# Performance work log

Measured on AMD Instinct MI355X. Metric: run time of the kernel, lower is better.

## Reference

```python
import jax, jax.numpy as jnp
import numpy as np

L, D, NH, DH, K = 2, 128, 4, 32, 3  # blocks, latent_dim, heads, head_dim, kernel

def _ln(x, eps=1e-6):
    mu = x.mean(-1, keepdims=True)
    var = x.var(-1, keepdims=True)
    return (x - mu) / jnp.sqrt(var + eps)

def setup_inputs() -> dict:
    key = jax.random.key(0)
    ks = jax.random.split(key, 12)
    B, Hd, Wd = 2, 64, 96
    s = 0.02
    p = lambda k, shape: jax.random.normal(k, shape, jnp.float32) * s
    return {
        'feat_map': jax.random.normal(ks[0], (B, D, Hd, Wd), jnp.float32),
        'feat_map_up': jax.random.normal(ks[1], (B, D, 2 * Hd, 2 * Wd), jnp.float32),
        'nc_w': jnp.ones((L, D), jnp.float32), 'nc_b': jnp.zeros((L, D), jnp.float32),
        'wq': p(ks[2], (L, D, D)), 'bq': jnp.zeros((L, D), jnp.float32),
        'wkv': p(ks[3], (L, D, 2 * D)), 'bkv': jnp.zeros((L, 2 * D), jnp.float32),
        'wo': p(ks[4], (L, D, D)), 'bo': jnp.zeros((L, D), jnp.float32),
        'w1': p(ks[5], (L, D, 4 * D)), 'b1': jnp.zeros((L, 4 * D), jnp.float32),
        'w2': p(ks[6], (L, 4 * D, D)), 'b2': jnp.zeros((L, D), jnp.float32),
        'wqf': p(ks[7], (D, D)), 'bqf': jnp.zeros((D,), jnp.float32),
        'wcf': p(ks[8], (D, D)), 'bcf': jnp.zeros((D,), jnp.float32),
        'upsample_factor': 2,
    }

def reference(feat_map, feat_map_up, nc_w, nc_b, wq, bq, wkv, bkv, wo, bo,
              w1, b1, w2, b2, wqf, bqf, wcf, bcf, upsample_factor):
    B, C, Hd, Wd = feat_map.shape
    Hu, Wu = Hd * upsample_factor, Wd * upsample_factor
    N = B * Hu * Wu
    # ---- local 3x3 context via replicate-pad + shifted slices (== pad+unfold) ----
    pad = jnp.pad(feat_map, ((0, 0), (0, 0), (1, 1), (1, 1)), mode='edge')
    patches = jnp.stack([pad[:, :, i:i + Hd, j:j + Wd]
                         for i in range(K) for j in range(K)], axis=2)  # [B,C,9,Hd,Wd]
    # nearest-neighbor upsample by factor (== F.interpolate nearest)
    patches = jnp.repeat(jnp.repeat(patches, upsample_factor, axis=-2),
                         upsample_factor, axis=-1)                      # [B,C,9,Hu,Wu]
    context = patches.transpose(0, 3, 4, 2, 1).reshape(N, K * K, C)     # [(b h w),9,C]
    x = feat_map_up.transpose(0, 2, 3, 1).reshape(N, 1, C)              # [(b h w),1,C]
    scale = 1.0 / float(np.sqrt(DH))
    for l in range(L):
        # cross-attn: x = x + Attn(norm1(x), norm_ctx(context))
        ctx_n = _ln(context) * nc_w[l] + nc_b[l]
        q = _ln(x) @ wq[l] + bq[l]
        kv = ctx_n @ wkv[l] + bkv[l]
        k_, v_ = kv[..., :D], kv[..., D:]
        qh = q.reshape(N, 1, NH, DH).transpose(0, 2, 1, 3)       # [N,h,1,dh]
        kh = k_.reshape(N, K * K, NH, DH).transpose(0, 2, 1, 3)  # [N,h,9,dh]
        vh = v_.reshape(N, K * K, NH, DH).transpose(0, 2, 1, 3)
        attn = jax.nn.softmax(jnp.einsum('nhqd,nhkd->nhqk', qh, kh) * scale, axis=-1)
        o = jnp.einsum('nhqk,nhkd->nhqd', attn, vh).transpose(0, 2, 1, 3).reshape(N, 1, D)
        x = x + (o @ wo[l] + bo[l])
        # MLP: x = x + W2 gelu(W1 norm2(x))
        h = jax.nn.gelu(_ln(x) @ w1[l] + b1[l])  # tanh-approx gelu
        x = x + (h @ w2[l] + b2[l])
    # ---- final query-context attention mask ----
    xq = _ln(x) @ wqf + bqf
    ctxp = _ln(context) @ wcf + bcf
    logits = jnp.einsum('nqc,nkc->nqk', xq, ctxp) * (1.0 / float(np.sqrt(D)))
    attn_mask = jax.nn.softmax(logits, axis=-1)              # [N,1,9]
    return attn_mask.reshape(B, Hu, Wu, K * K).transpose(0, 3, 1, 2)  # [B,9,Hu,Wu]
```

## Files before the change

kernel.cpp:

```cpp
#include <hip/hip_runtime.h>

namespace {

constexpr int THREADS = 256;
constexpr int HdC = 64, WdC = 96, HuC = 128, WuC = 192;


__device__ __forceinline__ float gelu_tanh(float x) {
  float z = 0.7978845608028654f * (x + 0.044715f * x * x * x);
  float e = __expf(2.0f * z);
  float t = 1.0f - 2.0f / (e + 1.0f);
  return 0.5f * x * (1.0f + t);
}

__device__ __forceinline__ unsigned short f2bf(float f) {
  unsigned int u = __builtin_bit_cast(unsigned int, f);
  u = (u + 0x7FFFu + ((u >> 16) & 1u)) >> 16;
  return (unsigned short)u;
}

__device__ __forceinline__ float bf2f(unsigned short u) {
  unsigned int x = ((unsigned int)u) << 16;
  return __builtin_bit_cast(float, x);
}
// ... 357 lines not shown
          FMA_ROW(xd + 0, a0, w);
          FMA_ROW(xd + 4, a1, w);
          FMA_ROW(xd + 8, a2, w);
          FMA_ROW(xd + 12, a3, w);
        }
      }
    }
    {
      const float4 bv = *reinterpret_cast<const float4*>(b2 + l * 128 + col0);
#pragma unroll
      for (int i = 0; i < 4; ++i) {
        float* xr = sm.xs + (row0 + i) * XS_S + col0;
        float4 x = *reinterpret_cast<float4*>(xr);
        x.x += xd[i * 4 + 0] + bv.x; x.y += xd[i * 4 + 1] + bv.y;
        x.z += xd[i * 4 + 2] + bv.z; x.w += xd[i * 4 + 3] + bv.w;
        *reinterpret_cast<float4*>(xr) = x;
      }
    }
    __syncthreads();
  }

  layernorm_x(sm.xs, sm.xnT, sm.scratch, tid);
  gemm32(wqf, 128, sm.xnT, sm.wbuf, tid, acc);
  {
    const float4 bv = *reinterpret_cast<const float4*>(bqf + col0);
#pragma unroll
    for (int i = 0; i < 4; ++i) {
      float4 o;
      o.x = acc[i * 4 + 0] + bv.x; o.y = acc[i * 4 + 1] + bv.y;
      o.z = acc[i * 4 + 2] + bv.z; o.w = acc[i * 4 + 3] + bv.w;
      *reinterpret_cast<float4*>(sm.outb + (row0 + i) * OB_S + col0) = o;
    }
  }
  gemm96<false>(wcf, 128, sm.ctxT, sm.wbuf, sm.kvb, bcf, nullptr, tid);
  __syncthreads();
  {
    const int px = tid >> 3, sub = tid & 7;
    const int lr = (((px >> 3) >> 1) << 2) | ((px & 7) >> 1);
    const float* qrow = sm.outb + px * OB_S;
    {
      const float* crow = sm.kvb + (lr * 9 + sub) * KV_S;
      float s = 0.f;
#pragma unroll 8
      for (int c = 0; c < 128; c += 4) {
        const float4 qv = *reinterpret_cast<const float4*>(qrow + c);
        const float4 cv = *reinterpret_cast<const float4*>(crow + c);
        s += qv.x * cv.x + qv.y * cv.y + qv.z * cv.z + qv.w * cv.w;
      }
      sm.scratch[SC_LG + px * 12 + sub] = s;
    }
    if (sub == 0) {
      const float* crow = sm.kvb + (lr * 9 + 8) * KV_S;
      float s = 0.f;
#pragma unroll 8
      for (int c = 0; c < 128; c += 4) {
        const float4 qv = *reinterpret_cast<const float4*>(qrow + c);
        const float4 cv = *reinterpret_cast<const float4*>(crow + c);
        s += qv.x * cv.x + qv.y * cv.y + qv.z * cv.z + qv.w * cv.w;
      }
      sm.scratch[SC_LG + px * 12 + 8] = s;
    }
  }
  __syncthreads();
  if (tid < 32) {
    const int px = tid;
    const int hu = hu0 + (px >> 3), wu = wu0 + (px & 7);
    float lg[9], mx = -1e30f;
#pragma unroll
    for (int kk = 0; kk < 9; ++kk) {
      lg[kk] = sm.scratch[SC_LG + px * 12 + kk] * 0.08838834764831845f;
      mx = fmaxf(mx, lg[kk]);
    }
    float sum = 0.f;
#pragma unroll
    for (int kk = 0; kk < 9; ++kk) { lg[kk] = __expf(lg[kk] - mx); sum += lg[kk]; }
    const float inv = 1.f / sum;
#pragma unroll
    for (int kk = 0; kk < 9; ++kk)
      out[((bz * 9 + kk) * HuC + hu) * WuC + wu] = lg[kk] * inv;
  }
}


constexpr int PANEL = 16384;
constexpr int N_PANELS = 26;
constexpr size_t WS_NEEDED = (size_t)N_PANELS * PANEL * 2 + 2048;
constexpr int CBS = 136;
constexpr int XTS = 132;

constexpr int MSC_ATT = 0;
constexpr int MSC_LN  = 1152;
constexpr int MSC_ST  = 1408;
constexpr int MSC_N   = 1472;

typedef __attribute__((ext_vector_type(8))) short bf16x8;
typedef __attribute__((ext_vector_type(4))) float f32x4;
typedef __attribute__((ext_vector_type(8))) unsigned short u16x8;

struct alignas(16) SmemM {
  unsigned short ctxn[80 * CBS];
  unsigned short kvb[80 * CBS];
  unsigned short xn[32 * CBS];
  unsigned short hb[32 * CBS];
  unsigned short outb[32 * CBS];
  float scratch[MSC_N];
};
static_assert(sizeof(SmemM) <= 80 * 1024, "LDS budget (need 2 blocks/CU)");

__global__ void prep_weights(
    const float* __restrict__ nc_w, const float* __restrict__ nc_b,
    const float* __restrict__ wq, const float* __restrict__ wkv,
    const float* __restrict__ bkv,
    const float* __restrict__ wo, const float* __restrict__ w1,
    const float* __restrict__ w2, const float* __restrict__ wqf,
    const float* __restrict__ wcf,
    unsigned short* __restrict__ wsp, float* __restrict__ wsb) {
  const int b = blockIdx.x;
  const int t = threadIdx.x;
  if (b >= 104) {
    const int l = b - 104;
    float acc = bkv[l * 256 + t];
    for (int k = 0; k < 128; ++k)
      acc += nc_b[l * 128 + k] * wkv[l * 32768 + k * 256 + t];
    wsb[l * 256 + t] = acc;
    return;
  }
  const int pid = b >> 2, qtr = b & 3;
  const float* src = wqf; int N = 128, koff = 0, noff = 0;
  const float* sc = nullptr;
  if (pid < 24) {
    const int l = pid / 12, loc = pid % 12;
    if (loc == 0)      { src = wq + l * 16384;  N = 128; }
    else if (loc == 1) { src = wkv + l * 32768; N = 256; sc = nc_w + l * 128; }
    else if (loc == 2) { src = wkv + l * 32768; N = 256; noff = 128; sc = nc_w + l * 128; }
    else if (loc == 3) { src = wo + l * 16384;  N = 128; }
    else if (loc < 8)  { src = w1 + l * 65536;  N = 512; noff = (loc - 4) * 128; }
    else               { src = w2 + l * 65536;  N = 128; koff = (loc - 8) * 128; }
  } else if (pid == 25) { src = wcf; }
  unsigned short* dst = wsp + pid * PANEL;
#pragma unroll
  for (int p = 0; p < 2; ++p) {
    const int e = t + p * 256;
    const int n = e & 127;
    const int kg = e >> 7;
    const int k0 = qtr * 32 + kg * 8;
    unsigned short tmp[8];
#pragma unroll
    for (int i = 0; i < 8; ++i) {
      const float s = sc ? sc[k0 + i] : 1.f;
      tmp[i] = f2bf(src[(k0 + i + koff) * N + noff + n] * s);
    }
    *reinterpret_cast<u16x8*>(dst + n * 128 + k0) = *reinterpret_cast<u16x8*>(tmp);
  }
}

__device__ __forceinline__ void load_b8(const unsigned short* __restrict__ W,
                                        bf16x8 b[2][4], int nl, int q8, int w2t) {
#pragma unroll
  for (int t = 0; t < 2; ++t)
#pragma unroll
    for (int ks = 0; ks < 4; ++ks)
      b[t][ks] = *reinterpret_cast<const bf16x8*>(
          W + ((w2t + t) * 16 + nl) * 128 + ks * 32 + q8);
}

__device__ __forceinline__ void mfma32v(const unsigned short* A, const bf16x8 b[2][4],
                                        f32x4 acc[4], int nl, int q8, bool init) {
  if (init) {
#pragma unroll
    for (int i = 0; i < 4; ++i) acc[i] = (f32x4){0.f, 0.f, 0.f, 0.f};
  }
#pragma unroll
  for (int ks = 0; ks < 4; ++ks) {
    const bf16x8 a0 = *reinterpret_cast<const bf16x8*>(A + nl * CBS + ks * 32 + q8);
    const bf16x8 a1 = *reinterpret_cast<const bf16x8*>(A + (16 + nl) * CBS + ks * 32 + q8);
    acc[0] = __builtin_amdgcn_mfma_f32_16x16x32_bf16(a0, b[0][ks], acc[0], 0, 0, 0);
    acc[1] = __builtin_amdgcn_mfma_f32_16x16x32_bf16(a0, b[1][ks], acc[1], 0, 0, 0);
    acc[2] = __builtin_amdgcn_mfma_f32_16x16x32_bf16(a1, b[0][ks], acc[2], 0, 0, 0);
    acc[3] = __builtin_amdgcn_mfma_f32_16x16x32_bf16(a1, b[1][ks], acc[3], 0, 0, 0);
  }
}

__device__ __forceinline__ void mfma72v(const unsigned short* Ctx, const bf16x8 b[2][4],
                                        f32x4 acc[10], int nl, int q8) {
#pragma unroll
  for (int i = 0; i < 10; ++i) acc[i] = (f32x4){0.f, 0.f, 0.f, 0.f};
#pragma unroll
  for (int ks = 0; ks < 4; ++ks) {
    const bf16x8 b0 = b[0][ks], b1 = b[1][ks];
#pragma unroll
    for (int rt = 0; rt < 5; ++rt) {
      const bf16x8 a = *reinterpret_cast<const bf16x8*>(
          Ctx + (rt * 16 + nl) * CBS + ks * 32 + q8);
      acc[rt * 2 + 0] = __builtin_amdgcn_mfma_f32_16x16x32_bf16(a, b0, acc[rt * 2 + 0], 0, 0, 0);
      acc[rt * 2 + 1] = __builtin_amdgcn_mfma_f32_16x16x32_bf16(a, b1, acc[rt * 2 + 1], 0, 0, 0);
    }
  }
}

__device__ __forceinline__ void ln_x(const float (&xr)[2][2][4], unsigned short* xn,
                                     float* scratch, int wave, int nl, int qm) {
#pragma unroll
  for (int rt = 0; rt < 2; ++rt)
#pragma unroll
    for (int r = 0; r < 4; ++r) {
      float s1 = xr[rt][0][r] + xr[rt][1][r];
      float s2 = xr[rt][0][r] * xr[rt][0][r] + xr[rt][1][r] * xr[rt][1][r];
#pragma unroll
      for (int m = 1; m < 16; m <<= 1) {
        s1 += __shfl_xor(s1, m, 64);
        s2 += __shfl_xor(s2, m, 64);
      }
      if (nl == 0) {
        const int px = rt * 16 + qm + r;
        scratch[MSC_LN + px * 4 + wave] = s1;
        scratch[MSC_LN + 128 + px * 4 + wave] = s2;
      }
    }
  __syncthreads();
#pragma unroll
  for (int rt = 0; rt < 2; ++rt)
#pragma unroll
    for (int r = 0; r < 4; ++r) {
      const int px = rt * 16 + qm + r;
      float a = 0.f, b = 0.f;
#pragma unroll
      for (int w = 0; w < 4; ++w) {
        a += scratch[MSC_LN + px * 4 + w];
        b += scratch[MSC_LN + 128 + px * 4 + w];
      }
      const float m = a * (1.f / 128.f);
      const float v = b * (1.f / 128.f) - m * m;
      const float rs = rsqrtf(v + 1e-6f);
#pragma unroll
      for (int t = 0; t < 2; ++t)
        xn[px * CBS + (wave * 2 + t) * 16 + nl] = f2bf((xr[rt][t][r] - m) * rs);
    }
  __syncthreads();
}

__global__ __launch_bounds__(THREADS, 2) void fused_interp_mfma(
    const float* __restrict__ fm, const float* __restrict__ fmu,
    const float* __restrict__ bq, const float* __restrict__ bo,
    const float* __restrict__ b1, const float* __restrict__ b2,
    const float* __restrict__ bqf, const float* __restrict__ bcf,
    const unsigned short* __restrict__ wsp, const float* __restrict__ wsb,
    float* __restrict__ out) {
  __shared__ SmemM sm;
  const int tid = threadIdx.x;
  const int bx = blockIdx.x, by = blockIdx.y, bz = blockIdx.z;
  const int lh0 = by * 2, lw0 = bx * 4;
  const int hu0 = by * 4, wu0 = bx * 8;

  const int lane = tid & 63;
  const int wave = tid >> 6;
  const int nl = lane & 15;
  const int q8 = (lane >> 4) * 8;
  const int qm = (lane >> 4) * 4;
  const int w2t = wave * 2;

  {
    float* xtmp = reinterpret_cast<float*>(sm.ctxn);
#pragma unroll
    for (int p = 0; p < 8; ++p) {
      const int e = tid + p * THREADS;
      const int pe = e & 15;
      const int c = e >> 4;
      const int hu = hu0 + (pe >> 2);
      const int wu = wu0 + (pe & 3) * 2;
      const float2 v = *reinterpret_cast<const float2*>(
          &fmu[((bz * 128 + c) * HuC + hu) * WuC + wu]);
      const int px = (pe >> 2) * 8 + (pe & 3) * 2;
      xtmp[px * XTS + c] = v.x;
      xtmp[(px + 1) * XTS + c] = v.y;
    }
  }
  __syncthreads();
  float xr[2][2][4];
  {
    const float* xtmp = reinterpret_cast<const float*>(sm.ctxn);
#pragma unroll
    for (int rt = 0; rt < 2; ++rt)
#pragma unroll
      for (int t = 0; t < 2; ++t)
#pragma unroll
        for (int r = 0; r < 4; ++r)
          xr[rt][t][r] = xtmp[(rt * 16 + qm + r) * XTS + (w2t + t) * 16 + nl];
  }
  __syncthreads();

  {
    float* patch = reinterpret_cast<float*>(sm.kvb);
#pragma unroll
    for (int p = 0; p < 12; ++p) {
      const int e = tid + p * THREADS;
      const int c = e / 24;
      const int rem = e - c * 24;
      const int hs_i = rem / 6;
      const int ws_i = rem - hs_i * 6;
      int hd = lh0 - 1 + hs_i; hd = hd < 0 ? 0 : (hd > HdC - 1 ? HdC - 1 : hd);
      int wd = lw0 - 1 + ws_i; wd = wd < 0 ? 0 : (wd > WdC - 1 ? WdC - 1 : wd);
      patch[(hs_i * 6 + ws_i) * XTS + c] = fm[((bz * 128 + c) * HdC + hd) * WdC + wd];
    }
  }
  __syncthreads();
  {
    const float* patch = reinterpret_cast<const float*>(sm.kvb);
    if (tid < 192) {
      const int pp = tid >> 3, part = tid & 7;
      float s1 = 0.f, s2 = 0.f;
#pragma unroll
      for (int i = 0; i < 16; ++i) {
        const float v = patch[pp * XTS + part * 16 + i];
        s1 += v; s2 += v * v;
      }
      sm.scratch[MSC_ATT + tid * 2 + 0] = s1;
      sm.scratch[MSC_ATT + tid * 2 + 1] = s2;
    }
    __syncthreads();
    if (tid < 24) {
      float a = 0.f, b = 0.f;
#pragma unroll
      for (int g = 0; g < 8; ++g) {
        a += sm.scratch[MSC_ATT + (tid * 8 + g) * 2 + 0];
        b += sm.scratch[MSC_ATT + (tid * 8 + g) * 2 + 1];
      }
      const float m = a * (1.f / 128.f);
      const float v = b * (1.f / 128.f) - m * m;
      sm.scratch[MSC_ST + tid * 2 + 0] = m;
      sm.scratch[MSC_ST + tid * 2 + 1] = rsqrtf(v + 1e-6f);
    }
    __syncthreads();
#pragma unroll
    for (int p = 0; p < 5; ++p) {
      const int e = tid + p * THREADS;
      if (e < 1152) {
        const int r = e >> 4, cg = e & 15;
        const int lr = r / 9;
        const int kk = r - lr * 9;
        const int ki = kk / 3, kj = kk - ki * 3;
        const int pp = ((lr >> 2) + ki) * 6 + (lr & 3) + kj;
        const float m = sm.scratch[MSC_ST + pp * 2 + 0];
        const float rs = sm.scratch[MSC_ST + pp * 2 + 1];
        unsigned short tmp[8];
#pragma unroll
        for (int j = 0; j < 8; ++j)
          tmp[j] = f2bf((patch[pp * XTS + cg * 8 + j] - m) * rs);
        *reinterpret_cast<u16x8*>(sm.ctxn + r * CBS + cg * 8) = *reinterpret_cast<u16x8*>(tmp);
      }
    }
  }
  __syncthreads();

  f32x4 acc4[4];
  f32x4 acc10[10];
  bf16x8 Ba[2][4], Bb[2][4];

  for (int l = 0; l < 2; ++l) {
    const unsigned short* P = wsp + (l * 12) * PANEL;

    float kb[2], vb[2], bqr[2], bor[2], b2r[2], b1r[4][2];
#pragma unroll
    for (int t = 0; t < 2; ++t) {
      const int n = (w2t + t) * 16 + nl;
      kb[t] = wsb[l * 256 + n];
      vb[t] = wsb[l * 256 + 128 + n];
      bqr[t] = bq[l * 128 + n];
      bor[t] = bo[l * 128 + n];
      b2r[t] = b2[l * 128 + n];
#pragma unroll
      for (int cc = 0; cc < 4; ++cc) b1r[cc][t] = b1[l * 512 + cc * 128 + n];
    }

    load_b8(P + 0 * PANEL, Ba, nl, q8, w2t);
    load_b8(P + 1 * PANEL, Bb, nl, q8, w2t);
    ln_x(xr, sm.xn, sm.scratch, wave, nl, qm);

    mfma32v(sm.xn, Ba, acc4, nl, q8, true);
#pragma unroll
    for (int rt = 0; rt < 2; ++rt)
#pragma unroll
      for (int t = 0; t < 2; ++t) {
        const int n = (w2t + t) * 16 + nl;
#pragma unroll
        for (int r = 0; r < 4; ++r)
          sm.outb[(rt * 16 + qm + r) * CBS + n] = f2bf(acc4[rt * 2 + t][r] + bqr[t]);
      }
    mfma72v(sm.ctxn, Bb, acc10, nl, q8);
    load_b8(P + 2 * PANEL, Ba, nl, q8, w2t);
#pragma unroll
    for (int t = 0; t < 2; ++t) {
      const int n = (w2t + t) * 16 + nl;
#pragma unroll
      for (int rt = 0; rt < 5; ++rt)
#pragma unroll
        for (int r = 0; r < 4; ++r) {
          const int row = rt * 16 + qm + r;
          if (row < 72) sm.kvb[row * CBS + n] = f2bf(acc10[rt * 2 + t][r] + kb[t]);
        }
    }
    __syncthreads();

    {
      const int u = tid >> 1, sub = tid & 1;
      const int px = u >> 2, h = u & 3;
      const int lr = (((px >> 3) >> 1) << 2) | ((px & 7) >> 1);
      const unsigned short* qrow = sm.outb + px * CBS + h * 32;
      const int base = sub ? 5 : 0;
      const int cnt = sub ? 4 : 5;
      float mine[5];
#pragma unroll
      for (int i = 0; i < 5; ++i) mine[i] = 0.f;
#pragma unroll
      for (int c8 = 0; c8 < 4; ++c8) {
        const u16x8 qa = *reinterpret_cast<const u16x8*>(qrow + c8 * 8);
        float qaf[8];
#pragma unroll
        for (int j = 0; j < 8; ++j) qaf[j] = bf2f(qa[j]);
#pragma unroll
        for (int i = 0; i < 5; ++i) {
          if (i < cnt) {
            const u16x8 ka = *reinterpret_cast<const u16x8*>(
                sm.kvb + (lr * 9 + base + i) * CBS + h * 32 + c8 * 8);
            float s = 0.f;
#pragma unroll
            for (int j = 0; j < 8; ++j) s += qaf[j] * bf2f(ka[j]);
            mine[i] += s;
          }
        }
      }
#pragma unroll
      for (int i = 0; i < 5; ++i) mine[i] *= 0.17677669529663687f;
      float other[5];
#pragma unroll
      for (int i = 0; i < 5; ++i) other[i] = __shfl_xor(mine[i], 1, 64);
      float lg[9];
#pragma unroll
      for (int j = 0; j < 5; ++j) lg[j] = sub ? other[j] : mine[j];
#pragma unroll
      for (int j = 0; j < 4; ++j) lg[5 + j] = sub ? mine[j] : other[j];
      float mx = -1e30f;
#pragma unroll
      for (int kk = 0; kk < 9; ++kk) mx = fmaxf(mx, lg[kk]);
      float sum = 0.f;
#pragma unroll
      for (int kk = 0; kk < 9; ++kk) { lg[kk] = __expf(lg[kk] - mx); sum += lg[kk]; }
      const float inv = 1.f / sum;
#pragma unroll
      for (int j = 0; j < 5; ++j)
        if (j < cnt) sm.scratch[MSC_ATT + (px * 4 + h) * 9 + base + j] = lg[base + j] * inv;
    }
    __syncthreads();

    mfma72v(sm.ctxn, Ba, acc10, nl, q8);
    load_b8(P + 3 * PANEL, Bb, nl, q8, w2t);
#pragma unroll
    for (int t = 0; t < 2; ++t) {
      const int n = (w2t + t) * 16 + nl;
#pragma unroll
      for (int rt = 0; rt < 5; ++rt)
#pragma unroll
        for (int r = 0; r < 4; ++r) {
          const int row = rt * 16 + qm + r;
          if (row < 72) sm.kvb[row * CBS + n] = f2bf(acc10[rt * 2 + t][r] + vb[t]);
        }
    }
    __syncthreads();

    {
      const int px = tid >> 3, cg = tid & 7, c0 = cg * 16;
      const int lr = (((px >> 3) >> 1) << 2) | ((px & 7) >> 1);
      const float* aw = sm.scratch + MSC_ATT + (px * 4 + (cg >> 1)) * 9;
      float o[16];
#pragma unroll
      for (int j = 0; j < 16; ++j) o[j] = 0.f;
#pragma unroll
      for (int kk = 0; kk < 9; ++kk) {
        const float a = aw[kk];
        const unsigned short* vrow = sm.kvb + (lr * 9 + kk) * CBS + c0;
        const u16x8 v0 = *reinterpret_cast<const u16x8*>(vrow);
        const u16x8 v1 = *reinterpret_cast<const u16x8*>(vrow + 8);
#pragma unroll
        for (int j = 0; j < 8; ++j) {
          o[j] += a * bf2f(v0[j]);
          o[8 + j] += a * bf2f(v1[j]);
        }
      }
      unsigned short tmp[16];
#pragma unroll
      for (int j = 0; j < 16; ++j) tmp[j] = f2bf(o[j]);
      *reinterpret_cast<u16x8*>(sm.xn + px * CBS + c0) = *reinterpret_cast<u16x8*>(tmp);
      *reinterpret_cast<u16x8*>(sm.xn + px * CBS + c0 + 8) = *reinterpret_cast<u16x8*>(tmp + 8);
    }
    __syncthreads();

    mfma32v(sm.xn, Bb, acc4, nl, q8, true);
#pragma unroll
    for (int rt = 0; rt < 2; ++rt)
#pragma unroll
      for (int t = 0; t < 2; ++t)
#pragma unroll
        for (int r = 0; r < 4; ++r)
          xr[rt][t][r] += acc4[rt * 2 + t][r] + bor[t];

    load_b8(P + 4 * PANEL, Ba, nl, q8, w2t);
    ln_x(xr, sm.xn, sm.scratch, wave, nl, qm);
    f32x4 xd[4];
    for (int cc = 0; cc < 4; ++cc) {
      mfma32v(sm.xn, Ba, acc4, nl, q8, true);
      load_b8(P + (8 + cc) * PANEL, Bb, nl, q8, w2t);
#pragma unroll
      for (int rt = 0; rt < 2; ++rt)
#pragma unroll
        for (int t = 0; t < 2; ++t) {
          const int n = (w2t + t) * 16 + nl;
#pragma unroll
          for (int r = 0; r < 4; ++r)
            sm.hb[(rt * 16 + qm + r) * CBS + n] =
                f2bf(gelu_tanh(acc4[rt * 2 + t][r] + b1r[cc][t]));
        }
      __syncthreads();
      if (cc < 3) load_b8(P + (5 + cc) * PANEL, Ba, nl, q8, w2t);
      mfma32v(sm.hb, Bb, xd, nl, q8, cc == 0);
      if (cc < 3) __syncthreads();
    }
#pragma unroll
    for (int rt = 0; rt < 2; ++rt)
#pragma unroll
      for (int t = 0; t < 2; ++t)
#pragma unroll
        for (int r = 0; r < 4; ++r)
          xr[rt][t][r] += xd[rt * 2 + t][r] + b2r[t];
  }

  float bqfr[2], bcfr[2];
#pragma unroll
  for (int t = 0; t < 2; ++t) {
    const int n = (w2t + t) * 16 + nl;
    bqfr[t] = bqf[n];
    bcfr[t] = bcf[n];
  }
  load_b8(wsp + 24 * PANEL, Ba, nl, q8, w2t);
  load_b8(wsp + 25 * PANEL, Bb, nl, q8, w2t);
  ln_x(xr, sm.xn, sm.scratch, wave, nl, qm);
  mfma32v(sm.xn, Ba, acc4, nl, q8, true);
#pragma unroll
  for (int rt = 0; rt < 2; ++rt)
#pragma unroll
    for (int t = 0; t < 2; ++t) {
      const int n = (w2t + t) * 16 + nl;
#pragma unroll
      for (int r = 0; r < 4; ++r)
        sm.outb[(rt * 16 + qm + r) * CBS + n] = f2bf(acc4[rt * 2 + t][r] + bqfr[t]);
    }
  mfma72v(sm.ctxn, Bb, acc10, nl, q8);
#pragma unroll
  for (int t = 0; t < 2; ++t) {
    const int n = (w2t + t) * 16 + nl;
#pragma unroll
    for (int rt = 0; rt < 5; ++rt)
#pragma unroll
      for (int r = 0; r < 4; ++r) {
        const int row = rt * 16 + qm + r;
        if (row < 72) sm.kvb[row * CBS + n] = f2bf(acc10[rt * 2 + t][r] + bcfr[t]);
      }
  }
  __syncthreads();
  {
    const int px = tid >> 3, sub = tid & 7;
    const int lr = (((px >> 3) >> 1) << 2) | ((px & 7) >> 1);
    const unsigned short* qrow = sm.outb + px * CBS;
#pragma unroll
    for (int which = 0; which < 2; ++which) {
      if (which == 1 && sub != 0) break;
      const int kk = (which == 0) ? sub : 8;
      const unsigned short* crow = sm.kvb + (lr * 9 + kk) * CBS;
      float s = 0.f;
#pragma unroll
      for (int c8 = 0; c8 < 16; ++c8) {
        const u16x8 qa = *reinterpret_cast<const u16x8*>(qrow + c8 * 8);
        const u16x8 ca = *reinterpret_cast<const u16x8*>(crow + c8 * 8);
#pragma unroll
        for (int j = 0; j < 8; ++j) s += bf2f(qa[j]) * bf2f(ca[j]);
      }
      sm.scratch[MSC_ATT + px * 12 + kk] = s;
    }
  }
  __syncthreads();
  if (tid < 32) {
    const int px = tid;
    const int hu = hu0 + (px >> 3), wu = wu0 + (px & 7);
    float lg[9], mx = -1e30f;
#pragma unroll
    for (int kk = 0; kk < 9; ++kk) {
      lg[kk] = sm.scratch[MSC_ATT + px * 12 + kk] * 0.08838834764831845f;
      mx = fmaxf(mx, lg[kk]);
    }
    float sum = 0.f;
#pragma unroll
    for (int kk = 0; kk < 9; ++kk) { lg[kk] = __expf(lg[kk] - mx); sum += lg[kk]; }
    const float inv = 1.f / sum;
#pragma unroll
    for (int kk = 0; kk < 9; ++kk)
      out[((bz * 9 + kk) * HuC + hu) * WuC + wu] = lg[kk] * inv;
  }
}

}

extern "C" void kernel_launch(void* const* d_in, const int* in_sizes, int n_in,
                              void* d_out, int out_size, void* d_ws, size_t ws_size,
                              hipStream_t stream) {
  const float* fm   = (const float*)d_in[0];
  const float* fmu  = (const float*)d_in[1];
  const float* nc_w = (const float*)d_in[2];
  const float* nc_b = (const float*)d_in[3];
  const float* wq   = (const float*)d_in[4];
  const float* bq   = (const float*)d_in[5];
  const float* wkv  = (const float*)d_in[6];
  const float* bkv  = (const float*)d_in[7];
  const float* wo   = (const float*)d_in[8];
  const float* bo   = (const float*)d_in[9];
  const float* w1   = (const float*)d_in[10];
  const float* b1   = (const float*)d_in[11];
  const float* w2   = (const float*)d_in[12];
  const float* b2   = (const float*)d_in[13];
  const float* wqf  = (const float*)d_in[14];
  const float* bqf  = (const float*)d_in[15];
  const float* wcf  = (const float*)d_in[16];
  const float* bcf  = (const float*)d_in[17];
  float* out = (float*)d_out;

  dim3 grid(24, 32, 2);
  if (ws_size >= WS_NEEDED) {
    unsigned short* wsp = (unsigned short*)d_ws;
    float* wsb = (float*)((char*)d_ws + (size_t)N_PANELS * PANEL * 2);
    prep_weights<<<dim3(106), dim3(256), 0, stream>>>(
        nc_w, nc_b, wq, wkv, bkv, wo, w1, w2, wqf, wcf, wsp, wsb);
    fused_interp_mfma<<<grid, dim3(THREADS), 0, stream>>>(
        fm, fmu, bq, bo, b1, b2, bqf, bcf, wsp, wsb, out);
  } else {
    fused_interp_kernel<<<grid, dim3(THREADS), 0, stream>>>(
        fm, fmu, nc_w, nc_b, wq, bq, wkv, bkv, wo, bo, w1, b1, w2, b2,
        wqf, bqf, wcf, bcf, out);
  }
}
```

Before: 305.5 us.

## Use 8 waves per block with one 16-column tile each in MFMA kernel

```diff
diff --git a/kernel.cpp b/kernel.cpp
--- a/kernel.cpp
+++ b/kernel.cpp
@@ -463,6 +463,7 @@
 }
 
 
+constexpr int TM = 512;
 constexpr int PANEL = 16384;
 constexpr int N_PANELS = 26;
 constexpr size_t WS_NEEDED = (size_t)N_PANELS * PANEL * 2 + 2048;
@@ -471,8 +472,9 @@
 
 constexpr int MSC_ATT = 0;
 constexpr int MSC_LN  = 1152;
-constexpr int MSC_ST  = 1408;
-constexpr int MSC_N   = 1472;
+constexpr int MSC_ST  = 1664;
+constexpr int MSC_MV  = 1712;
+constexpr int MSC_N   = 1776;
 
 typedef __attribute__((ext_vector_type(8))) short bf16x8;
 typedef __attribute__((ext_vector_type(4))) float f32x4;
@@ -535,58 +537,54 @@
   }
 }
 
-__device__ __forceinline__ void load_b8(const unsigned short* __restrict__ W,
-                                        bf16x8 b[2][4], int nl, int q8, int w2t) {
-#pragma unroll
-  for (int t = 0; t < 2; ++t)
-#pragma unroll
-    for (int ks = 0; ks < 4; ++ks)
-      b[t][ks] = *reinterpret_cast<const bf16x8*>(
-          W + ((w2t + t) * 16 + nl) * 128 + ks * 32 + q8);
-}
-
-__device__ __forceinline__ void mfma32v(const unsigned short* A, const bf16x8 b[2][4],
-                                        f32x4 acc[4], int nl, int q8, bool init) {
+__device__ __forceinline__ void load_b4(const unsigned short* __restrict__ W,
+                                        bf16x8 b[4], int nl, int q8, int wt) {
+#pragma unroll
+  for (int ks = 0; ks < 4; ++ks)
+    b[ks] = *reinterpret_cast<const bf16x8*>(
+        W + (wt * 16 + nl) * 128 + ks * 32 + q8);
+}
+
+__device__ __forceinline__ void mfma32s(const unsigned short* A, const bf16x8 b[4],
+                                        f32x4 acc[2], int nl, int q8, bool init) {
   if (init) {
-#pragma unroll
-    for (int i = 0; i < 4; ++i) acc[i] = (f32x4){0.f, 0.f, 0.f, 0.f};
+    acc[0] = (f32x4){0.f, 0.f, 0.f, 0.f};
+    acc[1] = (f32x4){0.f, 0.f, 0.f, 0.f};
   }
 #pragma unroll
   for (int ks = 0; ks < 4; ++ks) {
     const bf16x8 a0 = *reinterpret_cast<const bf16x8*>(A + nl * CBS + ks * 32 + q8);
     const bf16x8 a1 = *reinterpret_cast<const bf16x8*>(A + (16 + nl) * CBS + ks * 32 + q8);
-    acc[0] = __builtin_amdgcn_mfma_f32_16x16x32_bf16(a0, b[0][ks], acc[0], 0, 0, 0);
-    acc[1] = __builtin_amdgcn_mfma_f32_16x16x32_bf16(a0, b[1][ks], acc[1], 0, 0, 0);
-    acc[2] = __builtin_amdgcn_mfma_f32_16x16x32_bf16(a1, b[0][ks], acc[2], 0, 0, 0);
-    acc[3] = __builtin_amdgcn_mfma_f32_16x16x32_bf16(a1, b[1][ks], acc[3], 0, 0, 0);
-  }
-}
-
-__device__ __forceinline__ void mfma72v(const unsigned short* Ctx, const bf16x8 b[2][4],
-                                        f32x4 acc[10], int nl, int q8) {
-#pragma unroll
-  for (int i = 0; i < 10; ++i) acc[i] = (f32x4){0.f, 0.f, 0.f, 0.f};
+    acc[0] = __builtin_amdgcn_mfma_f32_16x16x32_bf16(a0, b[ks], acc[0], 0, 0, 0);
+    acc[1] = __builtin_amdgcn_mfma_f32_16x16x32_bf16(a1, b[ks], acc[1], 0, 0, 0);
+  }
+}
+
+__device__ __forceinline__ void mfma72s(const unsigned short* Ctx, const bf16x8 b[4],
+                                        f32x4 acc[5], int nl, int q8) {
+#pragma unroll
+  for (int i = 0; i < 5; ++i) acc[i] = (f32x4){0.f, 0.f, 0.f, 0.f};
 #pragma unroll
   for (int ks = 0; ks < 4; ++ks) {
-    const bf16x8 b0 = b[0][ks], b1 = b[1][ks];
+    const bf16x8 bk = b[ks];
 #pragma unroll
     for (int rt = 0; rt < 5; ++rt) {
       const bf16x8 a = *reinterpret_cast<const bf16x8*>(
           Ctx + (rt * 16 + nl) * CBS + ks * 32 + q8);
-      acc[rt * 2 + 0] = __builtin_amdgcn_mfma_f32_16x16x32_bf16(a, b0, acc[rt * 2 + 0], 0, 0, 0);
-      acc[rt * 2 + 1] = __builtin_amdgcn_mfma_f32_16x16x32_bf16(a, b1, acc[rt * 2 + 1], 0, 0, 0);
-    }
-  }
-}
-
-__device__ __forceinline__ void ln_x(const float (&xr)[2][2][4], unsigned short* xn,
-                                     float* scratch, int wave, int nl, int qm) {
+      acc[rt] = __builtin_amdgcn_mfma_f32_16x16x32_bf16(a, bk, acc[rt], 0, 0, 0);
+    }
+  }
+}
+
+__device__ __forceinline__ void ln_x8(const float (&xr)[2][4], unsigned short* xn,
+                                      float* scratch, int tid, int wave, int nl,
+                                      int qm, int n) {
 #pragma unroll
   for (int rt = 0; rt < 2; ++rt)
 #pragma unroll
     for (int r = 0; r < 4; ++r) {
-      float s1 = xr[rt][0][r] + xr[rt][1][r];
-      float s2 = xr[rt][0][r] * xr[rt][0][r] + xr[rt][1][r] * xr[rt][1][r];
+      float s1 = xr[rt][r];
+      float s2 = s1 * s1;
 #pragma unroll
       for (int m = 1; m < 16; m <<= 1) {
         s1 += __shfl_xor(s1, m, 64);
@@ -594,33 +592,37 @@
       }
       if (nl == 0) {
         const int px = rt * 16 + qm + r;
-        scratch[MSC_LN + px * 4 + wave] = s1;
-        scratch[MSC_LN + 128 + px * 4 + wave] = s2;
-      }
-    }
+        scratch[MSC_LN + px * 8 + wave] = s1;
+        scratch[MSC_LN + 256 + px * 8 + wave] = s2;
+      }
+    }
+  __syncthreads();
+  if (tid < 32) {
+    float a = 0.f, b = 0.f;
+#pragma unroll
+    for (int w = 0; w < 8; ++w) {
+      a += scratch[MSC_LN + tid * 8 + w];
+      b += scratch[MSC_LN + 256 + tid * 8 + w];
+    }
+    const float m = a * (1.f / 128.f);
+    const float v = b * (1.f / 128.f) - m * m;
+    scratch[MSC_MV + tid * 2 + 0] = m;
+    scratch[MSC_MV + tid * 2 + 1] = rsqrtf(v + 1e-6f);
+  }
   __syncthreads();
 #pragma unroll
   for (int rt = 0; rt < 2; ++rt)
 #pragma unroll
     for (int r = 0; r < 4; ++r) {
       const int px = rt * 16 + qm + r;
-      float a = 0.f, b = 0.f;
-#pragma unroll
-      for (int w = 0; w < 4; ++w) {
-        a += scratch[MSC_LN + px * 4 + w];
-        b += scratch[MSC_LN + 128 + px * 4 + w];
-      }
-      const float m = a * (1.f / 128.f);
-      const float v = b * (1.f / 128.f) - m * m;
-      const float rs = rsqrtf(v + 1e-6f);
-#pragma unroll
-      for (int t = 0; t < 2; ++t)
-        xn[px * CBS + (wave * 2 + t) * 16 + nl] = f2bf((xr[rt][t][r] - m) * rs);
-    }
-  __syncthreads();
-}
-
-__global__ __launch_bounds__(THREADS, 2) void fused_interp_mfma(
+      const float m = scratch[MSC_MV + px * 2 + 0];
+      const float rs = scratch[MSC_MV + px * 2 + 1];
+      xn[px * CBS + n] = f2bf((xr[rt][r] - m) * rs);
+    }
+  __syncthreads();
+}
+
+__global__ __launch_bounds__(TM, 4) void fused_interp_mfma(
     const float* __restrict__ fm, const float* __restrict__ fmu,
     const float* __restrict__ bq, const float* __restrict__ bo,
     const float* __restrict__ b1, const float* __restrict__ b2,
@@ -638,13 +640,14 @@
   const int nl = lane & 15;
   const int q8 = (lane >> 4) * 8;
   const int qm = (lane >> 4) * 4;
-  const int w2t = wave * 2;
+  const int wt = wave;
+  const int n = wt * 16 + nl;
 
   {
     float* xtmp = reinterpret_cast<float*>(sm.ctxn);
 #pragma unroll
-    for (int p = 0; p < 8; ++p) {
-      const int e = tid + p * THREADS;
+    for (int p = 0; p < 4; ++p) {
+      const int e = tid + p * TM;
       const int pe = e & 15;
       const int c = e >> 4;
       const int hu = hu0 + (pe >> 2);
@@ -657,24 +660,22 @@
     }
   }
   __syncthreads();
-  float xr[2][2][4];
+  float xr[2][4];
   {
     const float* xtmp = reinterpret_cast<const float*>(sm.ctxn);
 #pragma unroll
     for (int rt = 0; rt < 2; ++rt)
 #pragma unroll
-      for (int t = 0; t < 2; ++t)
-#pragma unroll
-        for (int r = 0; r < 4; ++r)
-          xr[rt][t][r] = xtmp[(rt * 16 + qm + r) * XTS + (w2t + t) * 16 + nl];
+      for (int r = 0; r < 4; ++r)
+        xr[rt][r] = xtmp[(rt * 16 + qm + r) * XTS + n];
   }
   __syncthreads();
 
   {
     float* patch = reinterpret_cast<float*>(sm.kvb);
 #pragma unroll
-    for (int p = 0; p < 12; ++p) {
-      const int e = tid + p * THREADS;
+    for (int p = 0; p < 6; ++p) {
+      const int e = tid + p * TM;
       const int c = e / 24;
       const int rem = e - c * 24;
       const int hs_i = rem / 6;
@@ -713,8 +714,8 @@
     }
     __syncthreads();
 #pragma unroll
-    for (int p = 0; p < 5; ++p) {
-      const int e = tid + p * THREADS;
+    for (int p = 0; p < 3; ++p) {
+      const int e = tid + p * TM;
       if (e < 1152) {
         const int r = e >> 4, cg = e & 15;
         const int lr = r / 9;
@@ -733,65 +734,53 @@
   }
   __syncthreads();
 
-  f32x4 acc4[4];
-  f32x4 acc10[10];
-  bf16x8 Ba[2][4], Bb[2][4];
+  f32x4 acc2[2];
+  f32x4 acc5[5];
+  bf16x8 Ba[4], Bb[4];
 
   for (int l = 0; l < 2; ++l) {
     const unsigned short* P = wsp + (l * 12) * PANEL;
 
-    float kb[2], vb[2], bqr[2], bor[2], b2r[2], b1r[4][2];
-#pragma unroll
-    for (int t = 0; t < 2; ++t) {
-      const int n = (w2t + t) * 16 + nl;
-      kb[t] = wsb[l * 256 + n];
-      vb[t] = wsb[l * 256 + 128 + n];
-      bqr[t] = bq[l * 128 + n];
-      bor[t] = bo[l * 128 + n];
-      b2r[t] = b2[l * 128 + n];
-#pragma unroll
-      for (int cc = 0; cc < 4; ++cc) b1r[cc][t] = b1[l * 512 + cc * 128 + n];
-    }
-
-    load_b8(P + 0 * PANEL, Ba, nl, q8, w2t);
-    load_b8(P + 1 * PANEL, Bb, nl, q8, w2t);
-    ln_x(xr, sm.xn, sm.scratch, wave, nl, qm);
-
-    mfma32v(sm.xn, Ba, acc4, nl, q8, true);
+    const float kb = wsb[l * 256 + n];
+    const float vb = wsb[l * 256 + 128 + n];
+    const float bqr = bq[l * 128 + n];
+    const float bor = bo[l * 128 + n];
+    const float b2r = b2[l * 128 + n];
+    float b1r[4];
+#pragma unroll
+    for (int cc = 0; cc < 4; ++cc) b1r[cc] = b1[l * 512 + cc * 128 + n];
+
+    load_b4(P + 0 * PANEL, Ba, nl, q8, wt);
+    load_b4(P + 1 * PANEL, Bb, nl, q8, wt);
+    ln_x8(xr, sm.xn, sm.scratch, tid, wave, nl, qm, n);
+
+    mfma32s(sm.xn, Ba, acc2, nl, q8, true);
 #pragma unroll
     for (int rt = 0; rt < 2; ++rt)
 #pragma unroll
-      for (int t = 0; t < 2; ++t) {
-        const int n = (w2t + t) * 16 + nl;
-#pragma unroll
-        for (int r = 0; r < 4; ++r)
-          sm.outb[(rt * 16 + qm + r) * CBS + n] = f2bf(acc4[rt * 2 + t][r] + bqr[t]);
-      }
-    mfma72v(sm.ctxn, Bb, acc10, nl, q8);
-    load_b8(P + 2 * PANEL, Ba, nl, q8, w2t);
-#pragma unroll
-    for (int t = 0; t < 2; ++t) {
-      const int n = (w2t + t) * 16 + nl;
-#pragma unroll
-      for (int rt = 0; rt < 5; ++rt)
-#pragma unroll
-        for (int r = 0; r < 4; ++r) {
-          const int row = rt * 16 + qm + r;
-          if (row < 72) sm.kvb[row * CBS + n] = f2bf(acc10[rt * 2 + t][r] + kb[t]);
-        }
-    }
+      for (int r = 0; r < 4; ++r)
+        sm.outb[(rt * 16 + qm + r) * CBS + n] = f2bf(acc2[rt][r] + bqr);
+    mfma72s(sm.ctxn, Bb, acc5, nl, q8);
+    load_b4(P + 2 * PANEL, Ba, nl, q8, wt);
+#pragma unroll
+    for (int rt = 0; rt < 5; ++rt)
+#pragma unroll
+      for (int r = 0; r < 4; ++r) {
+        const int row = rt * 16 + qm + r;
+        if (row < 72) sm.kvb[row * CBS + n] = f2bf(acc5[rt][r] + kb);
+      }
     __syncthreads();
 
     {
-      const int u = tid >> 1, sub = tid & 1;
+      const int u = tid >> 2, sub = tid & 3;
       const int px = u >> 2, h = u & 3;
       const int lr = (((px >> 3) >> 1) << 2) | ((px & 7) >> 1);
       const unsigned short* qrow = sm.outb + px * CBS + h * 32;
-      const int base = sub ? 5 : 0;
-      const int cnt = sub ? 4 : 5;
-      float mine[5];
-#pragma unroll
-      for (int i = 0; i < 5; ++i) mine[i] = 0.f;
+      const int base = (sub == 0) ? 0 : (1 + 2 * sub);
+      const int cnt = (sub == 0) ? 3 : 2;
+      float mine[3];
+#pragma unroll
+      for (int i = 0; i < 3; ++i) mine[i] = 0.f;
 #pragma unroll
       for (int c8 = 0; c8 < 4; ++c8) {
         const u16x8 qa = *reinterpret_cast<const u16x8*>(qrow + c8 * 8);
@@ -799,7 +788,7 @@
 #pragma unroll
         for (int j = 0; j < 8; ++j) qaf[j] = bf2f(qa[j]);
 #pragma unroll
-        for (int i = 0; i < 5; ++i) {
+        for (int i = 0; i < 3; ++i) {
           if (i < cnt) {
             const u16x8 ka = *reinterpret_cast<const u16x8*>(
                 sm.kvb + (lr * 9 + base + i) * CBS + h * 32 + c8 * 8);
@@ -810,152 +799,116 @@
           }
         }
       }
-#pragma unroll
-      for (int i = 0; i < 5; ++i) mine[i] *= 0.17677669529663687f;
-      float other[5];
-#pragma unroll
-      for (int i = 0; i < 5; ++i) other[i] = __shfl_xor(mine[i], 1, 64);
-      float lg[9];
-#pragma unroll
-      for (int j = 0; j < 5; ++j) lg[j] = sub ? other[j] : mine[j];
-#pragma unroll
-      for (int j = 0; j < 4; ++j) lg[5 + j] = sub ? mine[j] : other[j];
       float mx = -1e30f;
 #pragma unroll
-      for (int kk = 0; kk < 9; ++kk) mx = fmaxf(mx, lg[kk]);
+      for (int i = 0; i < 3; ++i) {
+        mine[i] *= 0.17677669529663687f;
+        if (i < cnt) mx = fmaxf(mx, mine[i]);
+      }
+      mx = fmaxf(mx, __shfl_xor(mx, 1, 64));
+      mx = fmaxf(mx, __shfl_xor(mx, 2, 64));
       float sum = 0.f;
 #pragma unroll
-      for (int kk = 0; kk < 9; ++kk) { lg[kk] = __expf(lg[kk] - mx); sum += lg[kk]; }
+      for (int i = 0; i < 3; ++i) {
+        if (i < cnt) { mine[i] = __expf(mine[i] - mx); sum += mine[i]; }
+      }
+      sum += __shfl_xor(sum, 1, 64);
+      sum += __shfl_xor(sum, 2, 64);
       const float inv = 1.f / sum;
 #pragma unroll
-      for (int j = 0; j < 5; ++j)
-        if (j < cnt) sm.scratch[MSC_ATT + (px * 4 + h) * 9 + base + j] = lg[base + j] * inv;
-    }
-    __syncthreads();
-
-    mfma72v(sm.ctxn, Ba, acc10, nl, q8);
-    load_b8(P + 3 * PANEL, Bb, nl, q8, w2t);
-#pragma unroll
-    for (int t = 0; t < 2; ++t) {
-      const int n = (w2t + t) * 16 + nl;
-#pragma unroll
-      for (int rt = 0; rt < 5; ++rt)
-#pragma unroll
-        for (int r = 0; r < 4; ++r) {
-          const int row = rt * 16 + qm + r;
-          if (row < 72) sm.kvb[row * CBS + n] = f2bf(acc10[rt * 2 + t][r] + vb[t]);
-        }
-    }
+      for (int i = 0; i < 3; ++i)
+        if (i < cnt) sm.scratch[MSC_ATT + (px * 4 + h) * 9 + base + i] = mine[i] * inv;
+    }
+    __syncthreads();
+
+    mfma72s(sm.ctxn, Ba, acc5, nl, q8);
+    load_b4(P + 3 * PANEL, Bb, nl, q8, wt);
+#pragma unroll
+    for (int rt = 0; rt < 5; ++rt)
+#pragma unroll
+      for (int r = 0; r < 4; ++r) {
+        const int row = rt * 16 + qm + r;
+        if (row < 72) sm.kvb[row * CBS + n] = f2bf(acc5[rt][r] + vb);
+      }
     __syncthreads();
 
     {
-      const int px = tid >> 3, cg = tid & 7, c0 = cg * 16;
+      const int px = tid >> 4, cg = tid & 15, c0 = cg * 8;
       const int lr = (((px >> 3) >> 1) << 2) | ((px & 7) >> 1);
-      const float* aw = sm.scratch + MSC_ATT + (px * 4 + (cg >> 1)) * 9;
-      float o[16];
-#pragma unroll
-      for (int j = 0; j < 16; ++j) o[j] = 0.f;
+      const float* aw = sm.scratch + MSC_ATT + (px * 4 + (cg >> 2)) * 9;
+      float o[8];
+#pragma unroll
+      for (int j = 0; j < 8; ++j) o[j] = 0.f;
 #pragma unroll
       for (int kk = 0; kk < 9; ++kk) {
         const float a = aw[kk];
-        const unsigned short* vrow = sm.kvb + (lr * 9 + kk) * CBS + c0;
-        const u16x8 v0 = *reinterpret_cast<const u16x8*>(vrow);
-        const u16x8 v1 = *reinterpret_cast<const u16x8*>(vrow + 8);
-#pragma unroll
-        for (int j = 0; j < 8; ++j) {
-          o[j] += a * bf2f(v0[j]);
-          o[8 + j] += a * bf2f(v1[j]);
-        }
-      }
-      unsigned short tmp[16];
-#pragma unroll
-      for (int j = 0; j < 16; ++j) tmp[j] = f2bf(o[j]);
+        const u16x8 v0 = *reinterpret_cast<const u16x8*>(sm.kvb + (lr * 9 + kk) * CBS + c0);
+#pragma unroll
+        for (int j = 0; j < 8; ++j) o[j] += a * bf2f(v0[j]);
+      }
+      unsigned short tmp[8];
+#pragma unroll
+      for (int j = 0; j < 8; ++j) tmp[j] = f2bf(o[j]);
       *reinterpret_cast<u16x8*>(sm.xn + px * CBS + c0) = *reinterpret_cast<u16x8*>(tmp);
-      *reinterpret_cast<u16x8*>(sm.xn + px * CBS + c0 + 8) = *reinterpret_cast<u16x8*>(tmp + 8);
-    }
-    __syncthreads();
-
-    mfma32v(sm.xn, Bb, acc4, nl, q8, true);
+    }
+    __syncthreads();
+
+    mfma32s(sm.xn, Bb, acc2, nl, q8, true);
 #pragma unroll
     for (int rt = 0; rt < 2; ++rt)
 #pragma unroll
-      for (int t = 0; t < 2; ++t)
+      for (int r = 0; r < 4; ++r)
+        xr[rt][r] += acc2[rt][r] + bor;
+
+    load_b4(P + 4 * PANEL, Ba, nl, q8, wt);
+    ln_x8(xr, sm.xn, sm.scratch, tid, wave, nl, qm, n);
+    f32x4 xd[2];
+    for (int cc = 0; cc < 4; ++cc) {
+      mfma32s(sm.xn, Ba, acc2, nl, q8, true);
+      load_b4(P + (8 + cc) * PANEL, Bb, nl, q8, wt);
+#pragma unroll
+      for (int rt = 0; rt < 2; ++rt)
 #pragma unroll
         for (int r = 0; r < 4; ++r)
-          xr[rt][t][r] += acc4[rt * 2 + t][r] + bor[t];
-
-    load_b8(P + 4 * PANEL, Ba, nl, q8, w2t);
-    ln_x(xr, sm.xn, sm.scratch, wave, nl, qm);
-    f32x4 xd[4];
-    for (int cc = 0; cc < 4; ++cc) {
-      mfma32v(sm.xn, Ba, acc4, nl, q8, true);
-      load_b8(P + (8 + cc) * PANEL, Bb, nl, q8, w2t);
-#pragma unroll
-      for (int rt = 0; rt < 2; ++rt)
-#pragma unroll
-        for (int t = 0; t < 2; ++t) {
-          const int n = (w2t + t) * 16 + nl;
-#pragma unroll
-          for (int r = 0; r < 4; ++r)
-            sm.hb[(rt * 16 + qm + r) * CBS + n] =
-                f2bf(gelu_tanh(acc4[rt * 2 + t][r] + b1r[cc][t]));
-        }
+          sm.hb[(rt * 16 + qm + r) * CBS + n] = f2bf(gelu_tanh(acc2[rt][r] + b1r[cc]));
       __syncthreads();
-      if (cc < 3) load_b8(P + (5 + cc) * PANEL, Ba, nl, q8, w2t);
-      mfma32v(sm.hb, Bb, xd, nl, q8, cc == 0);
+      if (cc < 3) load_b4(P + (5 + cc) * PANEL, Ba, nl, q8, wt);
+      mfma32s(sm.hb, Bb, xd, nl, q8, cc == 0);
       if (cc < 3) __syncthreads();
     }
 #pragma unroll
     for (int rt = 0; rt < 2; ++rt)
 #pragma unroll
-      for (int t = 0; t < 2; ++t)
-#pragma unroll
-        for (int r = 0; r < 4; ++r)
-          xr[rt][t][r] += xd[rt * 2 + t][r] + b2r[t];
-  }
-
-  float bqfr[2], bcfr[2];
-#pragma unroll
-  for (int t = 0; t < 2; ++t) {
-    const int n = (w2t + t) * 16 + nl;
-    bqfr[t] = bqf[n];
-    bcfr[t] = bcf[n];
-  }
-  load_b8(wsp + 24 * PANEL, Ba, nl, q8, w2t);
-  load_b8(wsp + 25 * PANEL, Bb, nl, q8, w2t);
-  ln_x(xr, sm.xn, sm.scratch, wave, nl, qm);
-  mfma32v(sm.xn, Ba, acc4, nl, q8, true);
+      for (int r = 0; r < 4; ++r)
+        xr[rt][r] += xd[rt][r] + b2r;
+  }
+
+  const float bqfr = bqf[n];
+  const float bcfr = bcf[n];
+  load_b4(wsp + 24 * PANEL, Ba, nl, q8, wt);
+  load_b4(wsp + 25 * PANEL, Bb, nl, q8, wt);
+  ln_x8(xr, sm.xn, sm.scratch, tid, wave, nl, qm, n);
+  mfma32s(sm.xn, Ba, acc2, nl, q8, true);
 #pragma unroll
   for (int rt = 0; rt < 2; ++rt)
 #pragma unroll
-    for (int t = 0; t < 2; ++t) {
-      const int n = (w2t + t) * 16 + nl;
-#pragma unroll
-      for (int r = 0; r < 4; ++r)
-        sm.outb[(rt * 16 + qm + r) * CBS + n] = f2bf(acc4[rt * 2 + t][r] + bqfr[t]);
-    }
-  mfma72v(sm.ctxn, Bb, acc10, nl, q8);
-#pragma unroll
-  for (int t = 0; t < 2; ++t) {
-    const int n = (w2t + t) * 16 + nl;
-#pragma unroll
-    for (int rt = 0; rt < 5; ++rt)
-#pragma unroll
-      for (int r = 0; r < 4; ++r) {
-        const int row = rt * 16 + qm + r;
-        if (row < 72) sm.kvb[row * CBS + n] = f2bf(acc10[rt * 2 + t][r] + bcfr[t]);
-      }
-  }
+    for (int r = 0; r < 4; ++r)
+      sm.outb[(rt * 16 + qm + r) * CBS + n] = f2bf(acc2[rt][r] + bqfr);
+  mfma72s(sm.ctxn, Bb, acc5, nl, q8);
+#pragma unroll
+  for (int rt = 0; rt < 5; ++rt)
+#pragma unroll
+    for (int r = 0; r < 4; ++r) {
+      const int row = rt * 16 + qm + r;
+      if (row < 72) sm.kvb[row * CBS + n] = f2bf(acc5[rt][r] + bcfr);
+    }
   __syncthreads();
   {
-    const int px = tid >> 3, sub = tid & 7;
-    const int lr = (((px >> 3) >> 1) << 2) | ((px & 7) >> 1);
-    const unsigned short* qrow = sm.outb + px * CBS;
-#pragma unroll
-    for (int which = 0; which < 2; ++which) {
-      if (which == 1 && sub != 0) break;
-      const int kk = (which == 0) ? sub : 8;
-      const unsigned short* crow = sm.kvb + (lr * 9 + kk) * CBS;
+    const int px = tid >> 4, sub = tid & 15;
+    if (sub < 9) {
+      const int lr = (((px >> 3) >> 1) << 2) | ((px & 7) >> 1);
+      const unsigned short* qrow = sm.outb + px * CBS;
+      const unsigned short* crow = sm.kvb + (lr * 9 + sub) * CBS;
       float s = 0.f;
 #pragma unroll
       for (int c8 = 0; c8 < 16; ++c8) {
@@ -964,7 +917,7 @@
 #pragma unroll
         for (int j = 0; j < 8; ++j) s += bf2f(qa[j]) * bf2f(ca[j]);
       }
-      sm.scratch[MSC_ATT + px * 12 + kk] = s;
+      sm.scratch[MSC_ATT + px * 12 + sub] = s;
     }
   }
   __syncthreads();
@@ -1018,7 +971,7 @@
     float* wsb = (float*)((char*)d_ws + (size_t)N_PANELS * PANEL * 2);
     prep_weights<<<dim3(106), dim3(256), 0, stream>>>(
         nc_w, nc_b, wq, wkv, bkv, wo, w1, w2, wqf, wcf, wsp, wsb);
-    fused_interp_mfma<<<grid, dim3(THREADS), 0, stream>>>(
+    fused_interp_mfma<<<grid, dim3(TM), 0, stream>>>(
         fm, fmu, bq, bo, b1, b2, bqf, bcf, wsp, wsb, out);
   } else {
     fused_interp_kernel<<<grid, dim3(THREADS), 0, stream>>>(
```

Result: slower. 349.4 us (+14.4%).

## Shrink LDS footprint by aliasing buffers to allow three blocks per CU

Applied to the files above, without the earlier changes.

```diff
diff --git a/kernel.cpp b/kernel.cpp
--- a/kernel.cpp
+++ b/kernel.cpp
@@ -470,23 +470,21 @@
 constexpr int XTS = 132;
 
 constexpr int MSC_ATT = 0;
-constexpr int MSC_LN  = 1152;
-constexpr int MSC_ST  = 1408;
-constexpr int MSC_N   = 1472;
+constexpr int MSC_LN  = 0;
+constexpr int MSC_ST  = 1152;
+constexpr int MSC_N   = 1200;
 
 typedef __attribute__((ext_vector_type(8))) short bf16x8;
 typedef __attribute__((ext_vector_type(4))) float f32x4;
 typedef __attribute__((ext_vector_type(8))) unsigned short u16x8;
 
 struct alignas(16) SmemM {
-  unsigned short ctxn[80 * CBS];
-  unsigned short kvb[80 * CBS];
+  unsigned short ctxn[72 * CBS];
+  unsigned short kvb[72 * CBS];
   unsigned short xn[32 * CBS];
-  unsigned short hb[32 * CBS];
-  unsigned short outb[32 * CBS];
   float scratch[MSC_N];
 };
-static_assert(sizeof(SmemM) <= 80 * 1024, "LDS budget (need 2 blocks/CU)");
+static_assert(sizeof(SmemM) <= 53248, "LDS budget (need 3 blocks/CU)");
 
 __global__ void prep_weights(
     const float* __restrict__ nc_w, const float* __restrict__ nc_b,
@@ -571,10 +569,29 @@
     const bf16x8 b0 = b[0][ks], b1 = b[1][ks];
 #pragma unroll
     for (int rt = 0; rt < 5; ++rt) {
+      const int rb = (rt < 4) ? rt * 16 : 56;
       const bf16x8 a = *reinterpret_cast<const bf16x8*>(
-          Ctx + (rt * 16 + nl) * CBS + ks * 32 + q8);
+          Ctx + (rb + nl) * CBS + ks * 32 + q8);
       acc[rt * 2 + 0] = __builtin_amdgcn_mfma_f32_16x16x32_bf16(a, b0, acc[rt * 2 + 0], 0, 0, 0);
       acc[rt * 2 + 1] = __builtin_amdgcn_mfma_f32_16x16x32_bf16(a, b1, acc[rt * 2 + 1], 0, 0, 0);
+    }
+  }
+}
+
+__device__ __forceinline__ void store72(unsigned short* kvb, const f32x4 acc[10],
+                                        const float bias[2], int nl, int qm, int w2t) {
+#pragma unroll
+  for (int t = 0; t < 2; ++t) {
+    const int n = (w2t + t) * 16 + nl;
+#pragma unroll
+    for (int rt = 0; rt < 5; ++rt) {
+      const int rb = (rt < 4) ? rt * 16 : 56;
+#pragma unroll
+      for (int r = 0; r < 4; ++r) {
+        const int row = rb + qm + r;
+        if (rt < 4 || qm + r >= 8)
+          kvb[row * CBS + n] = f2bf(acc[rt * 2 + t][r] + bias[t]);
+      }
     }
   }
 }
@@ -620,7 +637,7 @@
   __syncthreads();
 }
 
-__global__ __launch_bounds__(THREADS, 2) void fused_interp_mfma(
+__global__ __launch_bounds__(THREADS, 3) void fused_interp_mfma(
     const float* __restrict__ fm, const float* __restrict__ fmu,
     const float* __restrict__ bq, const float* __restrict__ bo,
     const float* __restrict__ b1, const float* __restrict__ b2,
@@ -758,6 +775,10 @@
     ln_x(xr, sm.xn, sm.scratch, wave, nl, qm);
 
     mfma32v(sm.xn, Ba, acc4, nl, q8, true);
+    mfma72v(sm.ctxn, Bb, acc10, nl, q8);
+    load_b8(P + 2 * PANEL, Ba, nl, q8, w2t);
+    store72(sm.kvb, acc10, kb, nl, qm, w2t);
+    __syncthreads();
 #pragma unroll
     for (int rt = 0; rt < 2; ++rt)
 #pragma unroll
@@ -765,28 +786,15 @@
         const int n = (w2t + t) * 16 + nl;
 #pragma unroll
         for (int r = 0; r < 4; ++r)
-          sm.outb[(rt * 16 + qm + r) * CBS + n] = f2bf(acc4[rt * 2 + t][r] + bqr[t]);
-      }
-    mfma72v(sm.ctxn, Bb, acc10, nl, q8);
-    load_b8(P + 2 * PANEL, Ba, nl, q8, w2t);
-#pragma unroll
-    for (int t = 0; t < 2; ++t) {
-      const int n = (w2t + t) * 16 + nl;
-#pragma unroll
-      for (int rt = 0; rt < 5; ++rt)
-#pragma unroll
-        for (int r = 0; r < 4; ++r) {
-          const int row = rt * 16 + qm + r;
-          if (row < 72) sm.kvb[row * CBS + n] = f2bf(acc10[rt * 2 + t][r] + kb[t]);
-        }
-    }
+          sm.xn[(rt * 16 + qm + r) * CBS + n] = f2bf(acc4[rt * 2 + t][r] + bqr[t]);
+      }
     __syncthreads();
 
     {
       const int u = tid >> 1, sub = tid & 1;
       const int px = u >> 2, h = u & 3;
       const int lr = (((px >> 3) >> 1) << 2) | ((px & 7) >> 1);
-      const unsigned short* qrow = sm.outb + px * CBS + h * 32;
+      const unsigned short* qrow = sm.xn + px * CBS + h * 32;
       const int base = sub ? 5 : 0;
       const int cnt = sub ? 4 : 5;
       float mine[5];
@@ -835,17 +843,7 @@
 
     mfma72v(sm.ctxn, Ba, acc10, nl, q8);
     load_b8(P + 3 * PANEL, Bb, nl, q8, w2t);
-#pragma unroll
-    for (int t = 0; t < 2; ++t) {
-      const int n = (w2t + t) * 16 + nl;
-#pragma unroll
-      for (int rt = 0; rt < 5; ++rt)
-#pragma unroll
-        for (int r = 0; r < 4; ++r) {
-          const int row = rt * 16 + qm + r;
-          if (row < 72) sm.kvb[row * CBS + n] = f2bf(acc10[rt * 2 + t][r] + vb[t]);
-        }
-    }
+    store72(sm.kvb, acc10, vb, nl, qm, w2t);
     __syncthreads();
 
     {
@@ -897,12 +895,12 @@
           const int n = (w2t + t) * 16 + nl;
 #pragma unroll
           for (int r = 0; r < 4; ++r)
-            sm.hb[(rt * 16 + qm + r) * CBS + n] =
+            sm.kvb[(rt * 16 + qm + r) * CBS + n] =
                 f2bf(gelu_tanh(acc4[rt * 2 + t][r] + b1r[cc][t]));
         }
       __syncthreads();
       if (cc < 3) load_b8(P + (5 + cc) * PANEL, Ba, nl, q8, w2t);
-      mfma32v(sm.hb, Bb, xd, nl, q8, cc == 0);
+      mfma32v(sm.kvb, Bb, xd, nl, q8, cc == 0);
       if (cc < 3) __syncthreads();
     }
 #pragma unroll
@@ -925,6 +923,9 @@
   load_b8(wsp + 25 * PANEL, Bb, nl, q8, w2t);
   ln_x(xr, sm.xn, sm.scratch, wave, nl, qm);
   mfma32v(sm.xn, Ba, acc4, nl, q8, true);
+  mfma72v(sm.ctxn, Bb, acc10, nl, q8);
+  store72(sm.kvb, acc10, bcfr, nl, qm, w2t);
+  __syncthreads();
 #pragma unroll
   for (int rt = 0; rt < 2; ++rt)
 #pragma unroll
@@ -932,25 +933,13 @@
       const int n = (w2t + t) * 16 + nl;
 #pragma unroll
       for (int r = 0; r < 4; ++r)
-        sm.outb[(rt * 16 + qm + r) * CBS + n] = f2bf(acc4[rt * 2 + t][r] + bqfr[t]);
-    }
-  mfma72v(sm.ctxn, Bb, acc10, nl, q8);
-#pragma unroll
-  for (int t = 0; t < 2; ++t) {
-    const int n = (w2t + t) * 16 + nl;
-#pragma unroll
-    for (int rt = 0; rt < 5; ++rt)
-#pragma unroll
-      for (int r = 0; r < 4; ++r) {
-        const int row = rt * 16 + qm + r;
-        if (row < 72) sm.kvb[row * CBS + n] = f2bf(acc10[rt * 2 + t][r] + bcfr[t]);
-      }
-  }
+        sm.xn[(rt * 16 + qm + r) * CBS + n] = f2bf(acc4[rt * 2 + t][r] + bqfr[t]);
+    }
   __syncthreads();
   {
     const int px = tid >> 3, sub = tid & 7;
     const int lr = (((px >> 3) >> 1) << 2) | ((px & 7) >> 1);
-    const unsigned short* qrow = sm.outb + px * CBS;
+    const unsigned short* qrow = sm.xn + px * CBS;
 #pragma unroll
     for (int which = 0; which < 2; ++which) {
       if (which == 1 && sub != 0) break;
```

New measurement: 393.7 us. +28.9%, slower.
